# Performance work log

Measured on AMD Instinct MI355X. Metric: run time of the kernel, lower is better.

The kernel has to match this reference:

```python
import jax, jax.numpy as jnp
import numpy as np

FOOT_Z = (2, 8)
SHANK_Z = (2, 8)
GYRO_LT = jnp.array([3, 4, 5])
GYRO_RT = jnp.array([9, 10, 11])
HF_BIN = 60  # int(30 * TS / SAMPLE_RATE) with TS=256, SAMPLE_RATE=128
EPS = 1e-6


def _std1(x, axis, keepdims=False):
    # torch .std uses unbiased estimator (ddof=1)
    return jnp.std(x, axis=axis, ddof=1, keepdims=keepdims)


def _var1(x, axis):
    return jnp.var(x, axis=axis, ddof=1)


def _kurtosis(x):
    mu = jnp.mean(x, axis=1, keepdims=True)
    std = jnp.clip(_std1(x, 1, keepdims=True), 1e-6, None)
    return jnp.clip(jnp.mean(((x - mu) / std) ** 4, axis=1), -10.0, 30.0)


def _skewness(x):
    mu = jnp.mean(x, axis=1, keepdims=True)
    std = jnp.clip(_std1(x, 1, keepdims=True), 1e-6, None)
    return jnp.clip(jnp.mean(((x - mu) / std) ** 3, axis=1), -10.0, 10.0)


def _zcr(x):
    signs = jnp.sign(x)
    signs = jnp.where(signs == 0, 1.0, signs)
    crosses = (signs[:, 1:] * signs[:, :-1] < 0).astype(jnp.float32)
    return jnp.mean(crosses, axis=1)


def _hf_ratio(x):
    power = jnp.abs(jnp.fft.rfft(x, axis=1)) ** 2  # [B, n_bins]
    total = jnp.sum(power, axis=1) + 1e-6
    hf = jnp.sum(power[:, HF_BIN:], axis=1)
    return hf / total


def _spectral_centroid(x):
    power = jnp.abs(jnp.fft.rfft(x, axis=1)) ** 2  # [B, n_bins]
    n_bins = power.shape[1]
    freqs = jnp.arange(n_bins, dtype=jnp.float32)
    centroid = jnp.sum(freqs * power, axis=1) / (jnp.sum(power, axis=1) + 1e-6)
    return centroid / n_bins


def _impact_duration(x, threshold=0.3):
    pk = jnp.max(jnp.abs(x), axis=1, keepdims=True)
    above = (jnp.abs(x) >= pk * threshold).astype(jnp.float32)
    return jnp.mean(above, axis=1)


def setup_inputs() -> dict:
    key = jax.random.key(0)
    k1, k2, k3 = jax.random.split(key, 3)
    B, C, T = 8192, 12, 256
    foot = jax.random.normal(k1, (B, C, T), jnp.float32)
    shank = jax.random.normal(k2, (B, C, T), jnp.float32)
    thigh = jax.random.normal(k3, (B, C, T), jnp.float32)
    return {"foot": foot, "shank": shank, "thigh": thigh}


def reference(foot, shank, thigh):
    fz_lt = foot[:, FOOT_Z[0], :]
    fz_rt = foot[:, FOOT_Z[1], :]
    sz_lt = shank[:, SHANK_Z[0], :]
    sz_rt = shank[:, SHANK_Z[1], :]

    f_pk_lt = jnp.max(jnp.abs(fz_lt), axis=1)
    f_pk_rt = jnp.max(jnp.abs(fz_rt), axis=1)
    s_pk_lt = jnp.max(jnp.abs(sz_lt), axis=1)
    s_pk_rt = jnp.max(jnp.abs(sz_rt), axis=1)

    ratio_lt = jnp.log1p(f_pk_lt / (s_pk_lt + 1e-4))
    ratio_rt = jnp.log1p(f_pk_rt / (s_pk_rt + 1e-4))

    hf_lt = _hf_ratio(fz_lt)
    hf_rt = _hf_ratio(fz_rt)

    std_lt = _std1(fz_lt, 1)
    std_rt = _std1(fz_rt, 1)

    T_half = fz_lt.shape[1] // 2
    decay_lt = jnp.mean(jnp.abs(fz_lt[:, :T_half]), axis=1) / (jnp.mean(jnp.abs(fz_lt[:, T_half:]), axis=1) + EPS)
    decay_rt = jnp.mean(jnp.abs(fz_rt[:, :T_half]), axis=1) / (jnp.mean(jnp.abs(fz_rt[:, T_half:]), axis=1) + EPS)

    vib_lt = jnp.mean(jnp.abs(sz_lt[:, 1:] - sz_lt[:, :-1]), axis=1)
    vib_rt = jnp.mean(jnp.abs(sz_rt[:, 1:] - sz_rt[:, :-1]), axis=1)

    var_ratio_lt = jnp.log1p(_var1(fz_lt, 1) / (_var1(sz_lt, 1) + 1e-4))
    var_ratio_rt = jnp.log1p(_var1(fz_rt, 1) / (_var1(sz_rt, 1) + 1e-4))

    sc_lt = _spectral_centroid(fz_lt)
    sc_rt = _spectral_centroid(fz_rt)
    dur_lt = _impact_duration(fz_lt)
    dur_rt = _impact_duration(fz_rt)

    fg_lt = foot[:, GYRO_LT, :]
    fg_rt = foot[:, GYRO_RT, :]
    fg_var_lt = jnp.log1p(jnp.sum(_var1(fg_lt, 2), axis=1))
    fg_var_rt = jnp.log1p(jnp.sum(_var1(fg_rt, 2), axis=1))
    fg_peak_lt = jnp.max(jnp.abs(fg_lt), axis=(1, 2))
    fg_peak_rt = jnp.max(jnp.abs(fg_rt), axis=(1, 2))

    sg_lt = shank[:, GYRO_LT, :]
    sg_rt = shank[:, GYRO_RT, :]
    sg_var_lt = jnp.log1p(jnp.sum(_var1(sg_lt, 2), axis=1))
    sg_var_rt = jnp.log1p(jnp.sum(_var1(sg_rt, 2), axis=1))
    sg_peak_lt = jnp.max(jnp.abs(sg_lt), axis=(1, 2))
    sg_peak_rt = jnp.max(jnp.abs(sg_rt), axis=(1, 2))

    tg_lt = thigh[:, GYRO_LT, :]
    tg_rt = thigh[:, GYRO_RT, :]
    tg_var_lt = jnp.log1p(jnp.sum(_var1(tg_lt, 2), axis=1))
    tg_var_rt = jnp.log1p(jnp.sum(_var1(tg_rt, 2), axis=1))
    tg_peak_lt = jnp.max(jnp.abs(tg_lt), axis=(1, 2))
    tg_peak_rt = jnp.max(jnp.abs(tg_rt), axis=(1, 2))

    asym_acc_lt = jnp.abs(f_pk_lt - s_pk_lt)
    asym_acc_rt = jnp.abs(f_pk_rt - s_pk_rt)
    asym_gy_lt = jnp.abs(fg_var_lt - sg_var_lt)
    asym_gy_rt = jnp.abs(fg_var_rt - sg_var_rt)

    foot_rms_lt = jnp.sqrt(jnp.mean(fz_lt ** 2, axis=1))
    foot_rms_rt = jnp.sqrt(jnp.mean(fz_rt ** 2, axis=1))
    shank_rms_lt = jnp.sqrt(jnp.mean(sz_lt ** 2, axis=1))
    shank_rms_rt = jnp.sqrt(jnp.mean(sz_rt ** 2, axis=1))
    trans_lt = jnp.log1p(shank_rms_lt / (foot_rms_lt + EPS))
    trans_rt = jnp.log1p(shank_rms_rt / (foot_rms_rt + EPS))

    kurt_lt = _kurtosis(fz_lt)
    kurt_rt = _kurtosis(fz_rt)
    skew_lt = _skewness(fz_lt)
    skew_rt = _skewness(fz_rt)
    zcr_lt = _zcr(fz_lt)
    zcr_rt = _zcr(fz_rt)

    return jnp.stack([
        f_pk_lt, f_pk_rt, s_pk_lt, s_pk_rt, ratio_lt, ratio_rt, hf_lt, hf_rt,
        std_lt, std_rt, decay_lt, decay_rt, vib_lt, vib_rt,
        var_ratio_lt, var_ratio_rt, sc_lt, sc_rt, dur_lt, dur_rt,
        fg_var_lt, fg_var_rt, fg_peak_lt, fg_peak_rt,
        sg_var_lt, sg_var_rt, sg_peak_lt, sg_peak_rt,
        tg_var_lt, tg_var_rt, tg_peak_lt, tg_peak_rt,
        asym_acc_lt, asym_acc_rt, asym_gy_lt, asym_gy_rt,
        trans_lt, trans_rt, kurt_lt, kurt_rt, skew_lt, skew_rt,
        zcr_lt, zcr_rt,
    ], axis=1)
```

## Files before the change

### kernel.cpp

```cpp
#include <hip/hip_runtime.h>
#include <math.h>


typedef __attribute__((ext_vector_type(8))) short short8;
typedef __attribute__((ext_vector_type(4))) float f32x4;

__device__ __forceinline__ float bcast63(float v){
  return __int_as_float(__builtin_amdgcn_readlane(__float_as_int(v), 63));
}
__device__ __forceinline__ float wsum(float v){
  v += __int_as_float(__builtin_amdgcn_update_dpp(0, __float_as_int(v), 0x111, 0xF, 0xF, true));
  v += __int_as_float(__builtin_amdgcn_update_dpp(0, __float_as_int(v), 0x112, 0xF, 0xF, true));
  v += __int_as_float(__builtin_amdgcn_update_dpp(0, __float_as_int(v), 0x114, 0xF, 0xF, true));
  v += __int_as_float(__builtin_amdgcn_update_dpp(0, __float_as_int(v), 0x118, 0xF, 0xF, true));
  v += __int_as_float(__builtin_amdgcn_update_dpp(0, __float_as_int(v), 0x142, 0xF, 0xF, true));
  v += __int_as_float(__builtin_amdgcn_update_dpp(0, __float_as_int(v), 0x143, 0xF, 0xF, true));
  return bcast63(v);
}
__device__ __forceinline__ float wmax(float v){
  v = fmaxf(v, __int_as_float(__builtin_amdgcn_update_dpp(0, __float_as_int(v), 0x111, 0xF, 0xF, true)));
  v = fmaxf(v, __int_as_float(__builtin_amdgcn_update_dpp(0, __float_as_int(v), 0x112, 0xF, 0xF, true)));
  v = fmaxf(v, __int_as_float(__builtin_amdgcn_update_dpp(0, __float_as_int(v), 0x114, 0xF, 0xF, true)));
  v = fmaxf(v, __int_as_float(__builtin_amdgcn_update_dpp(0, __float_as_int(v), 0x118, 0xF, 0xF, true)));
  v = fmaxf(v, __int_as_float(__builtin_amdgcn_update_dpp(0, __float_as_int(v), 0x142, 0xF, 0xF, true)));
  v = fmaxf(v, __int_as_float(__builtin_amdgcn_update_dpp(0, __float_as_int(v), 0x143, 0xF, 0xF, true)));
  return bcast63(v);
}
__device__ __forceinline__ float red16hi(float v){
  v += __int_as_float(__builtin_amdgcn_update_dpp(0, __float_as_int(v), 0x111, 0xF, 0xF, true));
  v += __int_as_float(__builtin_amdgcn_update_dpp(0, __float_as_int(v), 0x112, 0xF, 0xF, true));
  v += __int_as_float(__builtin_amdgcn_update_dpp(0, __float_as_int(v), 0x114, 0xF, 0xF, true));
  v += __int_as_float(__builtin_amdgcn_update_dpp(0, __float_as_int(v), 0x118, 0xF, 0xF, true));
  return v;
}
__device__ __forceinline__ float sum4(float4 v){ return (v.x+v.y)+(v.z+v.w); }
__device__ __forceinline__ float dot4(float4 v){ return (v.x*v.x+v.y*v.y)+(v.z*v.z+v.w*v.w); }
__device__ __forceinline__ float amax4(float4 v){ return fmaxf(fmaxf(fabsf(v.x),fabsf(v.y)),fmaxf(fabsf(v.z),fabsf(v.w))); }
__device__ __forceinline__ float asum4(float4 v){ return (fabsf(v.x)+fabsf(v.y))+(fabsf(v.z)+fabsf(v.w)); }
__device__ __forceinline__ float clampf(float v,float lo,float hi){ return fminf(fmaxf(v,lo),hi); }
__device__ __forceinline__ unsigned short f2bf(float f){
  unsigned u = __float_as_uint(f);
  return (unsigned short)((u + 0x7FFFu + ((u>>16)&1u)) >> 16);
}

__global__ __launch_bounds__(256) void build_trig(unsigned short* __restrict__ ws){
  int id   = blockIdx.x*256 + threadIdx.x;
  int lane = id & 63;
  int f    = (id>>6) & 1;
  int s    = (id>>7) & 7;
  int T    = (id>>10) & 7;
  int nb   = T*16 + (lane&15);
  int n0   = ((lane>>4)<<3) + (s<<5);
  short8 v;
  #pragma unroll
  for (int j=0;j<8;++j){
    int m = ((n0+j)*nb) & 255;
    if (f) m = (m+192)&255;
    v[j] = (short)f2bf(__cosf((float)m * 0.0245436926066f));
  }
  *(short8*)(ws + (size_t)id*8) = v;
}

__global__ __launch_bounds__(512,4) void biomech_kernel(
    const float* __restrict__ foot, const float* __restrict__ shank,
    const float* __restrict__ thigh, const unsigned short* __restrict__ ws,
    float* __restrict__ out, int B)
{
  const int t    = threadIdx.x;
  const int lane = t & 63;
  const int wv   = t >> 6;

  __shared__ __align__(16) unsigned short sA[16*256];
  __shared__ float sPart[8][16][3];
  __shared__ float sAlt[16];

  const long long b = (long long)blockIdx.x*8 + wv;
  if (b < B) {
    const float* fp = foot  + (size_t)b*3072;
    const float* sp = shank + (size_t)b*3072;
    const float* tp = thigh + (size_t)b*3072;

    float4 xl = ((const float4*)(fp+ 512))[lane];
    float4 xr = ((const float4*)(fp+2048))[lane];
    float4 yl = ((const float4*)(sp+ 512))[lane];
    float4 yr = ((const float4*)(sp+2048))[lane];
    float4 gv[6][3];
    #pragma unroll
    for (int g=0; g<6; ++g){
      const float* bse = (g<2)? fp : (g<4)? sp : tp;
      const float* src = bse + ((g&1)? 2304 : 768);
      gv[g][0] = ((const float4*)src      )[lane];
      gv[g][1] = ((const float4*)(src+256))[lane];
      gv[g][2] = ((const float4*)(src+512))[lane];
    }

    {
      int r0 = 2*wv, r1 = 2*wv+1;
      unsigned lo0 = (unsigned)f2bf(xl.x) | ((unsigned)f2bf(xl.y)<<16);
      unsigned hi0 = (unsigned)f2bf(xl.z) | ((unsigned)f2bf(xl.w)<<16);
      unsigned by0 = (((unsigned)r0<<9) + ((unsigned)lane<<3)) ^ (((unsigned)(r0&7))<<4);
      *(uint2*)((char*)sA + by0) = make_uint2(lo0,hi0);
      unsigned lo1 = (unsigned)f2bf(xr.x) | ((unsigned)f2bf(xr.y)<<16);
      unsigned hi1 = (unsigned)f2bf(xr.z) | ((unsigned)f2bf(xr.w)<<16);
      unsigned by1 = (((unsigned)r1<<9) + ((unsigned)lane<<3)) ^ (((unsigned)(r1&7))<<4);
      *(uint2*)((char*)sA + by1) = make_uint2(lo1,hi1);
    }

    float pk_l  = wmax(amax4(xl)), pk_r  = wmax(amax4(xr));
    float spk_l = wmax(amax4(yl)), spk_r = wmax(amax4(yr));
    float sum_l = wsum(sum4(xl)),  sum_r = wsum(sum4(xr));
    float sq_l  = wsum(dot4(xl)),  sq_r  = wsum(dot4(xr));
    float ssum_l= wsum(sum4(yl)),  ssum_r= wsum(sum4(yr));
    float ssq_l = wsum(dot4(yl)),  ssq_r = wsum(dot4(yr));
    float al = asum4(xl), ar = asum4(xr);
    float h1l = wsum(lane<32 ? al : 0.f), h2l = wsum(lane<32 ? 0.f : al);
    float h1r = wsum(lane<32 ? ar : 0.f), h2r = wsum(lane<32 ? 0.f : ar);
    float alt_l = wsum((xl.x - xl.y) + (xl.z - xl.w));
    float alt_r = wsum((xr.x - xr.y) + (xr.z - xr.w));
    if (lane == 0) { sAlt[2*wv] = alt_l; sAlt[2*wv+1] = alt_r; }

    float mu_l = sum_l*(1.f/256.f), mu_r = sum_r*(1.f/256.f);
    float var_fl = fmaxf((sq_l - 256.f*mu_l*mu_l)*(1.f/255.f), 0.f);
    float var_fr = fmaxf((sq_r - 256.f*mu_r*mu_r)*(1.f/255.f), 0.f);
    float std_l = sqrtf(var_fl), std_r = sqrtf(var_fr);
    float inv_l = 1.f/fmaxf(std_l,1e-6f), inv_r = 1.f/fmaxf(std_r,1e-6f);

    float p3l_c=0.f, p4l_c=0.f, p3r_c=0.f, p4r_c=0.f;
    {
      float p,p2;
      p=(xl.x-mu_l)*inv_l; p2=p*p; p3l_c+=p2*p; p4l_c+=p2*p2;
      p=(xl.y-mu_l)*inv_l; p2=p*p; p3l_c+=p2*p; p4l_c+=p2*p2;
      p=(xl.z-mu_l)*inv_l; p2=p*p; p3l_c+=p2*p; p4l_c+=p2*p2;
      p=(xl.w-mu_l)*inv_l; p2=p*p; p3l_c+=p2*p; p4l_c+=p2*p2;
      p=(xr.x-mu_r)*inv_r; p2=p*p; p3r_c+=p2*p; p4r_c+=p2*p2;
      p=(xr.y-mu_r)*inv_r; p2=p*p; p3r_c+=p2*p; p4r_c+=p2*p2;
      p=(xr.z-mu_r)*inv_r; p2=p*p; p3r_c+=p2*p; p4r_c+=p2*p2;
      p=(xr.w-mu_r)*inv_r; p2=p*p; p3r_c+=p2*p; p4r_c+=p2*p2;
    }
    float p3l = wsum(p3l_c), p4l = wsum(p4l_c);
    float p3r = wsum(p3r_c), p4r = wsum(p4r_c);

    float thr_l = 0.3f*pk_l, thr_r = 0.3f*pk_r;
    float dl_c = (fabsf(xl.x)>=thr_l?1.f:0.f) + (fabsf(xl.y)>=thr_l?1.f:0.f)
               + (fabsf(xl.z)>=thr_l?1.f:0.f) + (fabsf(xl.w)>=thr_l?1.f:0.f);
    float dr_c = (fabsf(xr.x)>=thr_r?1.f:0.f) + (fabsf(xr.y)>=thr_r?1.f:0.f)
               + (fabsf(xr.z)>=thr_r?1.f:0.f) + (fabsf(xr.w)>=thr_r?1.f:0.f);
    float dur_l = wsum(dl_c), dur_r = wsum(dr_c);

    float nxl = __shfl_down(xl.x,1), nxr = __shfl_down(xr.x,1);
    float nyl = __shfl_down(yl.x,1), nyr = __shfl_down(yr.x,1);
    const bool lastl = (lane==63);
    float zl_c = ((xl.x<0.f)!=(xl.y<0.f)?1.f:0.f) + ((xl.y<0.f)!=(xl.z<0.f)?1.f:0.f)
               + ((xl.z<0.f)!=(xl.w<0.f)?1.f:0.f)
               + ((!lastl && ((xl.w<0.f)!=(nxl<0.f)))?1.f:0.f);
    float zr_c = ((xr.x<0.f)!=(xr.y<0.f)?1.f:0.f) + ((xr.y<0.f)!=(xr.z<0.f)?1.f:0.f)
               + ((xr.z<0.f)!=(xr.w<0.f)?1.f:0.f)
               + ((!lastl && ((xr.w<0.f)!=(nxr<0.f)))?1.f:0.f);
    float zc_l = wsum(zl_c), zc_r = wsum(zr_c);
    float vl_c = fabsf(yl.y-yl.x)+fabsf(yl.z-yl.y)+fabsf(yl.w-yl.z) + (lastl?0.f:fabsf(nyl-yl.w));
    float vr_c = fabsf(yr.y-yr.x)+fabsf(yr.z-yr.y)+fabsf(yr.w-yr.z) + (lastl?0.f:fabsf(nyr-yr.w));
    float vib_l = wsum(vl_c), vib_r = wsum(vr_c);

    float gvar[6], gpk[6];
    #pragma unroll
    for (int g=0; g<6; ++g){
      float s0 = wsum(sum4(gv[g][0]));
      float s1 = wsum(sum4(gv[g][1]));
      float s2 = wsum(sum4(gv[g][2]));
      float qt = wsum(dot4(gv[g][0])+dot4(gv[g][1])+dot4(gv[g][2]));
      gpk[g]   = wmax(fmaxf(amax4(gv[g][0]),fmaxf(amax4(gv[g][1]),amax4(gv[g][2]))));
      gvar[g]  = (qt - (s0*s0+s1*s1+s2*s2)*(1.f/256.f))*(1.f/255.f);
    }

    float var_sl = fmaxf((ssq_l - ssum_l*ssum_l*(1.f/256.f))*(1.f/255.f), 0.f);
    float var_sr = fmaxf((ssq_r - ssum_r*ssum_r*(1.f/256.f))*(1.f/255.f), 0.f);
    float frms_l = sqrtf(sq_l *(1.f/256.f)), frms_r = sqrtf(sq_r *(1.f/256.f));
    float srms_l = sqrtf(ssq_l*(1.f/256.f)), srms_r = sqrtf(ssq_r*(1.f/256.f));
    float fgv_l = log1pf(gvar[0]), fgv_r = log1pf(gvar[1]);
    float sgv_l = log1pf(gvar[2]), sgv_r = log1pf(gvar[3]);
    float tgv_l = log1pf(gvar[4]), tgv_r = log1pf(gvar[5]);

    if (lane == 0) {
      float* o = out + (size_t)b*44;
      float4 v0 = {pk_l, pk_r, spk_l, spk_r};
      float2 v4 = {log1pf(pk_l/(spk_l+1e-4f)), log1pf(pk_r/(spk_r+1e-4f))};
      float4 v8 = {std_l, std_r,
                   (h1l*(1.f/128.f))/(h2l*(1.f/128.f)+1e-6f),
                   (h1r*(1.f/128.f))/(h2r*(1.f/128.f)+1e-6f)};
      float4 v12 = {vib_l*(1.f/255.f), vib_r*(1.f/255.f),
                    log1pf(var_fl/(var_sl+1e-4f)), log1pf(var_fr/(var_sr+1e-4f))};
      float2 v18 = {dur_l*(1.f/256.f), dur_r*(1.f/256.f)};
      float4 v20 = {fgv_l, fgv_r, gpk[0], gpk[1]};
      float4 v24 = {sgv_l, sgv_r, gpk[2], gpk[3]};
      float4 v28 = {tgv_l, tgv_r, gpk[4], gpk[5]};
      float4 v32 = {fabsf(pk_l-spk_l), fabsf(pk_r-spk_r),
                    fabsf(fgv_l-sgv_l), fabsf(fgv_r-sgv_r)};
      float4 v36 = {log1pf(srms_l/(frms_l+1e-6f)), log1pf(srms_r/(frms_r+1e-6f)),
                    clampf(p4l*(1.f/256.f), -10.f, 30.f), clampf(p4r*(1.f/256.f), -10.f, 30.f)};
      float4 v40 = {clampf(p3l*(1.f/256.f), -10.f, 10.f), clampf(p3r*(1.f/256.f), -10.f, 10.f),
                    zc_l*(1.f/255.f), zc_r*(1.f/255.f)};
      *(float4*)(o+0)  = v0;  *(float2*)(o+4)  = v4;
      *(float4*)(o+8)  = v8;  *(float4*)(o+12) = v12;
      *(float2*)(o+18) = v18; *(float4*)(o+20) = v20;
      *(float4*)(o+24) = v24; *(float4*)(o+28) = v28;
      *(float4*)(o+32) = v32; *(float4*)(o+36) = v36;
      *(float4*)(o+40) = v40;
    }
  }

  const int col = lane & 15;
  const int g16 = lane >> 4;
  const int T   = wv;
  const short8* ws8 = (const short8*)ws;
  short8 bc0 = ws8[((T*8+0)*2+0)*64 + lane];
  short8 bs0 = ws8[((T*8+0)*2+1)*64 + lane];
  short8 bc1 = ws8[((T*8+1)*2+0)*64 + lane];
  short8 bs1 = ws8[((T*8+1)*2+1)*64 + lane];
  __syncthreads();

  {
    f32x4 ac={0,0,0,0}, as={0,0,0,0};
    #pragma unroll
    for (int s=0; s<8; ++s){
      unsigned abyte = (((unsigned)col<<9) + ((unsigned)g16<<4) + ((unsigned)s<<6))
                       ^ (((unsigned)(col&7))<<4);
      short8 af = *(const short8*)((const char*)sA + abyte);
      short8 bcn, bsn;
      if (s < 6) {
        bcn = ws8[((T*8+s+2)*2+0)*64 + lane];
        bsn = ws8[((T*8+s+2)*2+1)*64 + lane];
      }
      ac = __builtin_amdgcn_mfma_f32_16x16x32_bf16(af, bc0, ac, 0,0,0);
      as = __builtin_amdgcn_mfma_f32_16x16x32_bf16(af, bs0, as, 0,0,0);
      bc0 = bc1; bs0 = bs1;
      if (s < 6) { bc1 = bcn; bs1 = bsn; }
    }

    float kf = (float)(T*16 + col);
    #pragma unroll
    for (int q=0; q<4; ++q){
      int row = (g16<<2) + q;
      float P = ac[q]*ac[q] + as[q]*as[q];
      float tp = red16hi(P);
      float cp = red16hi(kf*P);
      float hp;
      if (T == 3)      hp = red16hi(col >= 12 ? P : 0.f);
      else if (T >= 4) hp = tp;
      else             hp = 0.f;
      if (col == 15) {
        sPart[T][row][0]=tp; sPart[T][row][1]=hp; sPart[T][row][2]=cp;
      }
    }
  }
  __syncthreads();

  if (t < 16) {
    const int row = t;
    const long long bb = (long long)blockIdx.x*8 + (row>>1);
    if (bb < B) {
      float tot=0.f, hp=0.f, cw=0.f;
      #pragma unroll
      for (int tl=0; tl<8; ++tl){
        tot += sPart[tl][row][0];
        hp  += sPart[tl][row][1];
        cw  += sPart[tl][row][2];
      }
      float a = sAlt[row], P128 = a*a;
      tot += P128; hp += P128; cw = fmaf(128.f, P128, cw);
      int ch = row & 1;
      float* o = out + (size_t)bb*44;
      o[6+ch]  = hp/(tot+1e-6f);
      o[16+ch] = cw/(tot+1e-6f)*(1.f/129.f);
    }
  }
}

extern "C" void kernel_launch(void* const* d_in, const int* in_sizes, int n_in,
                              void* d_out, int out_size, void* d_ws, size_t ws_size,
                              hipStream_t stream) {
  const float* foot  = (const float*)d_in[0];
  const float* shank = (const float*)d_in[1];
  const float* thigh = (const float*)d_in[2];
  float* out = (float*)d_out;
  unsigned short* ws = (unsigned short*)d_ws;
  int B = in_sizes[0] / (12 * 256);
  build_trig<<<dim3(32), dim3(256), 0, stream>>>(ws);
  biomech_kernel<<<dim3((B+7)/8), dim3(512), 0, stream>>>(foot, shank, thigh, ws, out, B);
}
```

Before: 52.18 us.

## Defer readlane broadcasts and normalize skew/kurtosis moments in lane 63

Most wave reductions now leave their result in lane 63 instead of broadcasting it with readlane, and the scalar epilogue moves into lane 63. Skewness and kurtosis are computed from raw central moments and scaled by powers of 1/std afterwards. This removes the dependency of the moment loop on the std reduction and cuts many readlane broadcasts. The launch bound minimum occupancy drops from 4 to 2, which gives the compiler more registers per thread but may lower occupancy.

After: 66.11 us. +26.7%, slower.

```diff
diff --git a/kernel.cpp b/kernel.cpp
--- a/kernel.cpp
+++ b/kernel.cpp
@@ -5,32 +5,40 @@
 typedef __attribute__((ext_vector_type(8))) short short8;
 typedef __attribute__((ext_vector_type(4))) float f32x4;
 
-__device__ __forceinline__ float bcast63(float v){
+__device__ __forceinline__ float rdl63(float v){
   return __int_as_float(__builtin_amdgcn_readlane(__float_as_int(v), 63));
 }
+template<int CTL>
+__device__ __forceinline__ float dpp_step_sum(float v){
+  return v + __int_as_float(__builtin_amdgcn_update_dpp(0, __float_as_int(v), CTL, 0xF, 0xF, true));
+}
+template<int CTL>
+__device__ __forceinline__ float dpp_step_max(float v){
+  return fmaxf(v, __int_as_float(__builtin_amdgcn_update_dpp(0, __float_as_int(v), CTL, 0xF, 0xF, true)));
+}
 __device__ __forceinline__ float wsum(float v){
-  v += __int_as_float(__builtin_amdgcn_update_dpp(0, __float_as_int(v), 0x111, 0xF, 0xF, true));
-  v += __int_as_float(__builtin_amdgcn_update_dpp(0, __float_as_int(v), 0x112, 0xF, 0xF, true));
-  v += __int_as_float(__builtin_amdgcn_update_dpp(0, __float_as_int(v), 0x114, 0xF, 0xF, true));
-  v += __int_as_float(__builtin_amdgcn_update_dpp(0, __float_as_int(v), 0x118, 0xF, 0xF, true));
-  v += __int_as_float(__builtin_amdgcn_update_dpp(0, __float_as_int(v), 0x142, 0xF, 0xF, true));
-  v += __int_as_float(__builtin_amdgcn_update_dpp(0, __float_as_int(v), 0x143, 0xF, 0xF, true));
-  return bcast63(v);
+  v = dpp_step_sum<0x111>(v); v = dpp_step_sum<0x112>(v); v = dpp_step_sum<0x114>(v);
+  v = dpp_step_sum<0x118>(v); v = dpp_step_sum<0x142>(v); v = dpp_step_sum<0x143>(v);
+  return rdl63(v);
+}
+__device__ __forceinline__ float wsum63(float v){
+  v = dpp_step_sum<0x111>(v); v = dpp_step_sum<0x112>(v); v = dpp_step_sum<0x114>(v);
+  v = dpp_step_sum<0x118>(v); v = dpp_step_sum<0x142>(v); v = dpp_step_sum<0x143>(v);
+  return v;
 }
 __device__ __forceinline__ float wmax(float v){
-  v = fmaxf(v, __int_as_float(__builtin_amdgcn_update_dpp(0, __float_as_int(v), 0x111, 0xF, 0xF, true)));
-  v = fmaxf(v, __int_as_float(__builtin_amdgcn_update_dpp(0, __float_as_int(v), 0x112, 0xF, 0xF, true)));
-  v = fmaxf(v, __int_as_float(__builtin_amdgcn_update_dpp(0, __float_as_int(v), 0x114, 0xF, 0xF, true)));
-  v = fmaxf(v, __int_as_float(__builtin_amdgcn_update_dpp(0, __float_as_int(v), 0x118, 0xF, 0xF, true)));
-  v = fmaxf(v, __int_as_float(__builtin_amdgcn_update_dpp(0, __float_as_int(v), 0x142, 0xF, 0xF, true)));
-  v = fmaxf(v, __int_as_float(__builtin_amdgcn_update_dpp(0, __float_as_int(v), 0x143, 0xF, 0xF, true)));
-  return bcast63(v);
+  v = dpp_step_max<0x111>(v); v = dpp_step_max<0x112>(v); v = dpp_step_max<0x114>(v);
+  v = dpp_step_max<0x118>(v); v = dpp_step_max<0x142>(v); v = dpp_step_max<0x143>(v);
+  return rdl63(v);
+}
+__device__ __forceinline__ float wmax63(float v){
+  v = dpp_step_max<0x111>(v); v = dpp_step_max<0x112>(v); v = dpp_step_max<0x114>(v);
+  v = dpp_step_max<0x118>(v); v = dpp_step_max<0x142>(v); v = dpp_step_max<0x143>(v);
+  return v;
 }
 __device__ __forceinline__ float red16hi(float v){
-  v += __int_as_float(__builtin_amdgcn_update_dpp(0, __float_as_int(v), 0x111, 0xF, 0xF, true));
-  v += __int_as_float(__builtin_amdgcn_update_dpp(0, __float_as_int(v), 0x112, 0xF, 0xF, true));
-  v += __int_as_float(__builtin_amdgcn_update_dpp(0, __float_as_int(v), 0x114, 0xF, 0xF, true));
-  v += __int_as_float(__builtin_amdgcn_update_dpp(0, __float_as_int(v), 0x118, 0xF, 0xF, true));
+  v = dpp_step_sum<0x111>(v); v = dpp_step_sum<0x112>(v);
+  v = dpp_step_sum<0x114>(v); v = dpp_step_sum<0x118>(v);
   return v;
 }
 __device__ __forceinline__ float sum4(float4 v){ return (v.x+v.y)+(v.z+v.w); }
@@ -61,7 +69,7 @@
   *(short8*)(ws + (size_t)id*8) = v;
 }
 
-__global__ __launch_bounds__(512,4) void biomech_kernel(
+__global__ __launch_bounds__(512,2) void biomech_kernel(
     const float* __restrict__ foot, const float* __restrict__ shank,
     const float* __restrict__ thigh, const unsigned short* __restrict__ ws,
     float* __restrict__ out, int B)
@@ -107,45 +115,41 @@
     }
 
     float pk_l  = wmax(amax4(xl)), pk_r  = wmax(amax4(xr));
-    float spk_l = wmax(amax4(yl)), spk_r = wmax(amax4(yr));
+    float spk_l = wmax63(amax4(yl)), spk_r = wmax63(amax4(yr));
     float sum_l = wsum(sum4(xl)),  sum_r = wsum(sum4(xr));
-    float sq_l  = wsum(dot4(xl)),  sq_r  = wsum(dot4(xr));
-    float ssum_l= wsum(sum4(yl)),  ssum_r= wsum(sum4(yr));
-    float ssq_l = wsum(dot4(yl)),  ssq_r = wsum(dot4(yr));
+    float sq_l  = wsum63(dot4(xl)),  sq_r  = wsum63(dot4(xr));
+    float ssum_l= wsum63(sum4(yl)),  ssum_r= wsum63(sum4(yr));
+    float ssq_l = wsum63(dot4(yl)),  ssq_r = wsum63(dot4(yr));
     float al = asum4(xl), ar = asum4(xr);
-    float h1l = wsum(lane<32 ? al : 0.f), h2l = wsum(lane<32 ? 0.f : al);
-    float h1r = wsum(lane<32 ? ar : 0.f), h2r = wsum(lane<32 ? 0.f : ar);
-    float alt_l = wsum((xl.x - xl.y) + (xl.z - xl.w));
-    float alt_r = wsum((xr.x - xr.y) + (xr.z - xr.w));
-    if (lane == 0) { sAlt[2*wv] = alt_l; sAlt[2*wv+1] = alt_r; }
+    float h1l = wsum63(lane<32 ? al : 0.f), h2l = wsum63(lane<32 ? 0.f : al);
+    float h1r = wsum63(lane<32 ? ar : 0.f), h2r = wsum63(lane<32 ? 0.f : ar);
+    float alt_l = wsum63((xl.x - xl.y) + (xl.z - xl.w));
+    float alt_r = wsum63((xr.x - xr.y) + (xr.z - xr.w));
+    if (lane == 63) { sAlt[2*wv] = alt_l; sAlt[2*wv+1] = alt_r; }
 
     float mu_l = sum_l*(1.f/256.f), mu_r = sum_r*(1.f/256.f);
-    float var_fl = fmaxf((sq_l - 256.f*mu_l*mu_l)*(1.f/255.f), 0.f);
-    float var_fr = fmaxf((sq_r - 256.f*mu_r*mu_r)*(1.f/255.f), 0.f);
-    float std_l = sqrtf(var_fl), std_r = sqrtf(var_fr);
-    float inv_l = 1.f/fmaxf(std_l,1e-6f), inv_r = 1.f/fmaxf(std_r,1e-6f);
 
     float p3l_c=0.f, p4l_c=0.f, p3r_c=0.f, p4r_c=0.f;
     {
       float p,p2;
-      p=(xl.x-mu_l)*inv_l; p2=p*p; p3l_c+=p2*p; p4l_c+=p2*p2;
-      p=(xl.y-mu_l)*inv_l; p2=p*p; p3l_c+=p2*p; p4l_c+=p2*p2;
-      p=(xl.z-mu_l)*inv_l; p2=p*p; p3l_c+=p2*p; p4l_c+=p2*p2;
-      p=(xl.w-mu_l)*inv_l; p2=p*p; p3l_c+=p2*p; p4l_c+=p2*p2;
-      p=(xr.x-mu_r)*inv_r; p2=p*p; p3r_c+=p2*p; p4r_c+=p2*p2;
-      p=(xr.y-mu_r)*inv_r; p2=p*p; p3r_c+=p2*p; p4r_c+=p2*p2;
-      p=(xr.z-mu_r)*inv_r; p2=p*p; p3r_c+=p2*p; p4r_c+=p2*p2;
-      p=(xr.w-mu_r)*inv_r; p2=p*p; p3r_c+=p2*p; p4r_c+=p2*p2;
-    }
-    float p3l = wsum(p3l_c), p4l = wsum(p4l_c);
-    float p3r = wsum(p3r_c), p4r = wsum(p4r_c);
+      p=xl.x-mu_l; p2=p*p; p3l_c+=p2*p; p4l_c+=p2*p2;
+      p=xl.y-mu_l; p2=p*p; p3l_c+=p2*p; p4l_c+=p2*p2;
+      p=xl.z-mu_l; p2=p*p; p3l_c+=p2*p; p4l_c+=p2*p2;
+      p=xl.w-mu_l; p2=p*p; p3l_c+=p2*p; p4l_c+=p2*p2;
+      p=xr.x-mu_r; p2=p*p; p3r_c+=p2*p; p4r_c+=p2*p2;
+      p=xr.y-mu_r; p2=p*p; p3r_c+=p2*p; p4r_c+=p2*p2;
+      p=xr.z-mu_r; p2=p*p; p3r_c+=p2*p; p4r_c+=p2*p2;
+      p=xr.w-mu_r; p2=p*p; p3r_c+=p2*p; p4r_c+=p2*p2;
+    }
+    float p3l = wsum63(p3l_c), p4l = wsum63(p4l_c);
+    float p3r = wsum63(p3r_c), p4r = wsum63(p4r_c);
 
     float thr_l = 0.3f*pk_l, thr_r = 0.3f*pk_r;
     float dl_c = (fabsf(xl.x)>=thr_l?1.f:0.f) + (fabsf(xl.y)>=thr_l?1.f:0.f)
                + (fabsf(xl.z)>=thr_l?1.f:0.f) + (fabsf(xl.w)>=thr_l?1.f:0.f);
     float dr_c = (fabsf(xr.x)>=thr_r?1.f:0.f) + (fabsf(xr.y)>=thr_r?1.f:0.f)
                + (fabsf(xr.z)>=thr_r?1.f:0.f) + (fabsf(xr.w)>=thr_r?1.f:0.f);
-    float dur_l = wsum(dl_c), dur_r = wsum(dr_c);
+    float dur_l = wsum63(dl_c), dur_r = wsum63(dr_c);
 
     float nxl = __shfl_down(xl.x,1), nxr = __shfl_down(xr.x,1);
     float nyl = __shfl_down(yl.x,1), nyr = __shfl_down(yr.x,1);
@@ -156,31 +160,38 @@
     float zr_c = ((xr.x<0.f)!=(xr.y<0.f)?1.f:0.f) + ((xr.y<0.f)!=(xr.z<0.f)?1.f:0.f)
                + ((xr.z<0.f)!=(xr.w<0.f)?1.f:0.f)
                + ((!lastl && ((xr.w<0.f)!=(nxr<0.f)))?1.f:0.f);
-    float zc_l = wsum(zl_c), zc_r = wsum(zr_c);
+    float zc_l = wsum63(zl_c), zc_r = wsum63(zr_c);
     float vl_c = fabsf(yl.y-yl.x)+fabsf(yl.z-yl.y)+fabsf(yl.w-yl.z) + (lastl?0.f:fabsf(nyl-yl.w));
     float vr_c = fabsf(yr.y-yr.x)+fabsf(yr.z-yr.y)+fabsf(yr.w-yr.z) + (lastl?0.f:fabsf(nyr-yr.w));
-    float vib_l = wsum(vl_c), vib_r = wsum(vr_c);
+    float vib_l = wsum63(vl_c), vib_r = wsum63(vr_c);
 
     float gvar[6], gpk[6];
     #pragma unroll
     for (int g=0; g<6; ++g){
-      float s0 = wsum(sum4(gv[g][0]));
-      float s1 = wsum(sum4(gv[g][1]));
-      float s2 = wsum(sum4(gv[g][2]));
-      float qt = wsum(dot4(gv[g][0])+dot4(gv[g][1])+dot4(gv[g][2]));
-      gpk[g]   = wmax(fmaxf(amax4(gv[g][0]),fmaxf(amax4(gv[g][1]),amax4(gv[g][2]))));
+      float s0 = wsum63(sum4(gv[g][0]));
+      float s1 = wsum63(sum4(gv[g][1]));
+      float s2 = wsum63(sum4(gv[g][2]));
+      float qt = wsum63(dot4(gv[g][0])+dot4(gv[g][1])+dot4(gv[g][2]));
+      gpk[g]   = wmax63(fmaxf(amax4(gv[g][0]),fmaxf(amax4(gv[g][1]),amax4(gv[g][2]))));
       gvar[g]  = (qt - (s0*s0+s1*s1+s2*s2)*(1.f/256.f))*(1.f/255.f);
     }
 
-    float var_sl = fmaxf((ssq_l - ssum_l*ssum_l*(1.f/256.f))*(1.f/255.f), 0.f);
-    float var_sr = fmaxf((ssq_r - ssum_r*ssum_r*(1.f/256.f))*(1.f/255.f), 0.f);
-    float frms_l = sqrtf(sq_l *(1.f/256.f)), frms_r = sqrtf(sq_r *(1.f/256.f));
-    float srms_l = sqrtf(ssq_l*(1.f/256.f)), srms_r = sqrtf(ssq_r*(1.f/256.f));
-    float fgv_l = log1pf(gvar[0]), fgv_r = log1pf(gvar[1]);
-    float sgv_l = log1pf(gvar[2]), sgv_r = log1pf(gvar[3]);
-    float tgv_l = log1pf(gvar[4]), tgv_r = log1pf(gvar[5]);
-
-    if (lane == 0) {
+    if (lane == 63) {
+      float var_fl = fmaxf((sq_l - 256.f*mu_l*mu_l)*(1.f/255.f), 0.f);
+      float var_fr = fmaxf((sq_r - 256.f*mu_r*mu_r)*(1.f/255.f), 0.f);
+      float std_l = sqrtf(var_fl), std_r = sqrtf(var_fr);
+      float inv_l = 1.f/fmaxf(std_l,1e-6f), inv_r = 1.f/fmaxf(std_r,1e-6f);
+      float i2l = inv_l*inv_l, i2r = inv_r*inv_r;
+      float sk_l = p3l*i2l*inv_l*(1.f/256.f), sk_r = p3r*i2r*inv_r*(1.f/256.f);
+      float ku_l = p4l*i2l*i2l*(1.f/256.f),   ku_r = p4r*i2r*i2r*(1.f/256.f);
+      float var_sl = fmaxf((ssq_l - ssum_l*ssum_l*(1.f/256.f))*(1.f/255.f), 0.f);
+      float var_sr = fmaxf((ssq_r - ssum_r*ssum_r*(1.f/256.f))*(1.f/255.f), 0.f);
+      float frms_l = sqrtf(sq_l *(1.f/256.f)), frms_r = sqrtf(sq_r *(1.f/256.f));
+      float srms_l = sqrtf(ssq_l*(1.f/256.f)), srms_r = sqrtf(ssq_r*(1.f/256.f));
+      float fgv_l = log1pf(gvar[0]), fgv_r = log1pf(gvar[1]);
+      float sgv_l = log1pf(gvar[2]), sgv_r = log1pf(gvar[3]);
+      float tgv_l = log1pf(gvar[4]), tgv_r = log1pf(gvar[5]);
+
       float* o = out + (size_t)b*44;
       float4 v0 = {pk_l, pk_r, spk_l, spk_r};
       float2 v4 = {log1pf(pk_l/(spk_l+1e-4f)), log1pf(pk_r/(spk_r+1e-4f))};
@@ -196,8 +207,8 @@
       float4 v32 = {fabsf(pk_l-spk_l), fabsf(pk_r-spk_r),
                     fabsf(fgv_l-sgv_l), fabsf(fgv_r-sgv_r)};
       float4 v36 = {log1pf(srms_l/(frms_l+1e-6f)), log1pf(srms_r/(frms_r+1e-6f)),
-                    clampf(p4l*(1.f/256.f), -10.f, 30.f), clampf(p4r*(1.f/256.f), -10.f, 30.f)};
-      float4 v40 = {clampf(p3l*(1.f/256.f), -10.f, 10.f), clampf(p3r*(1.f/256.f), -10.f, 10.f),
+                    clampf(ku_l, -10.f, 30.f), clampf(ku_r, -10.f, 30.f)};
+      float4 v40 = {clampf(sk_l, -10.f, 10.f), clampf(sk_r, -10.f, 10.f),
                     zc_l*(1.f/255.f), zc_r*(1.f/255.f)};
       *(float4*)(o+0)  = v0;  *(float2*)(o+4)  = v4;
       *(float4*)(o+8)  = v8;  *(float4*)(o+12) = v12;
```
